# Kernel tuning notes

Hardware: AMD Instinct MI355X
Metric: run time of the kernel (lower is better)

Reference implementation:

```python
import jax, jax.numpy as jnp
import numpy as np

B, N, H = 32, 256, 1024
HEADS, NHID = 8, 128
NCLS = 7
BAND = 24
ALPHA = 0.2          # GAT leaky-relu slope
NEG = -9e15          # masked-attention fill, as in pyGAT


def setup_inputs() -> dict:
    key = jax.random.key(0)
    ks = jax.random.split(key, 16)
    def nrm(k, shp, s=0.02):
        return jax.random.normal(k, shp, dtype=jnp.float32) * s
    hidden_cls = jax.random.normal(ks[0], (B, N, H), dtype=jnp.float32)
    hidden_emo = jax.random.normal(ks[1], (B, N, H), dtype=jnp.float32)
    # causal band cliques, diagonal included (GAT uses clique - eye)
    t = jnp.arange(N)
    band = ((t[None, :] <= t[:, None]) & (t[None, :] > t[:, None] - BAND)).astype(jnp.float32)
    clique = jnp.broadcast_to(band, (B, N, N))
    labels = jax.random.randint(ks[2], (B, N), 0, NCLS)
    pooler_W = nrm(ks[3], (H, H)); pooler_b = jnp.zeros((H,), jnp.float32)
    gat_W = nrm(ks[4], (HEADS, H, NHID))
    gat_a1 = nrm(ks[5], (HEADS, NHID)); gat_a2 = nrm(ks[6], (HEADS, NHID))
    out_W = nrm(ks[7], (H, H))            # heads*nhid == H -> nclass=H
    out_a1 = nrm(ks[8], (H,)); out_a2 = nrm(ks[9], (H,))
    lin1_W = nrm(ks[10], (H, H)); lin1_b = jnp.zeros((H,), jnp.float32)
    lin0_W = nrm(ks[11], (2 * H, H)); lin0_b = jnp.zeros((H,), jnp.float32)
    cls_W = nrm(ks[12], (H, NCLS)); cls_b = jnp.zeros((NCLS,), jnp.float32)
    A = jax.random.uniform(ks[13], (NCLS, NCLS), dtype=jnp.float32) + 0.1
    hmm_A = A / A.sum(axis=1, keepdims=True)   # row-stochastic transition matrix
    return dict(hidden_cls=hidden_cls, hidden_emo=hidden_emo, clique=clique,
                labels=labels, pooler_W=pooler_W, pooler_b=pooler_b,
                gat_W=gat_W, gat_a1=gat_a1, gat_a2=gat_a2,
                out_W=out_W, out_a1=out_a1, out_a2=out_a2,
                lin1_W=lin1_W, lin1_b=lin1_b, lin0_W=lin0_W, lin0_b=lin0_b,
                cls_W=cls_W, cls_b=cls_b, hmm_A=hmm_A)


def _lrelu(x):
    return jnp.where(x > 0, x, ALPHA * x)


def reference(hidden_cls, hidden_emo, clique, labels, pooler_W, pooler_b,
              gat_W, gat_a1, gat_a2, out_W, out_a1, out_a2,
              lin1_W, lin1_b, lin0_W, lin0_b, cls_W, cls_b, hmm_A):
    # PoolerAll: dense + tanh on all token states (dropout = identity in eval)
    fea_cls = jnp.tanh(hidden_cls @ pooler_W + pooler_b)   # [B,N,H] (CLS per utt)
    fea_emo = jnp.tanh(hidden_emo @ pooler_W + pooler_b)   # [B,N,H] (mask tok per utt)

    eyeN = jnp.eye(N, dtype=clique.dtype)
    adjm = (clique - eyeN) > 0                             # [B,N,N] GAT adjacency

    def gat_one(x, am):                                    # x [N,H], am [N,N]
        Wh = jnp.einsum('nf,hfd->hnd', x, gat_W)           # [heads,N,nhid]
        e = _lrelu(jnp.einsum('hnd,hd->hn', Wh, gat_a1)[:, :, None]
                   + jnp.einsum('hnd,hd->hn', Wh, gat_a2)[:, None, :])
        att = jax.nn.softmax(jnp.where(am[None], e, NEG), axis=-1)
        h1 = jax.nn.elu(jnp.einsum('hnm,hmd->hnd', att, Wh))
        h1 = jnp.transpose(h1, (1, 0, 2)).reshape(N, HEADS * NHID)
        Wh2 = h1 @ out_W                                   # out attention layer (concat=False)
        e2 = _lrelu((Wh2 @ out_a1)[:, None] + (Wh2 @ out_a2)[None, :])
        h2 = jax.nn.softmax(jnp.where(am, e2, NEG), axis=-1) @ Wh2
        return jax.nn.elu(h2)                              # [N,H]

    gat_out = jax.vmap(gat_one)(fea_cls, adjm)             # [B,N,H]
    # row 0 replaced by (dropout of) fea_cls row 0, as in the original
    g = jnp.concatenate([fea_cls[:, :1], gat_out[:, 1:]], axis=1)
    g = jnp.concatenate([fea_cls, g @ lin1_W + lin1_b], axis=-1) @ lin0_W + lin0_b
    log_gat = jax.nn.softmax(g @ cls_W + cls_b, axis=-1)   # [B,N,NCLS] (probs)

    # HMM emission probs hmm_B(fea) = softmax(classifier(fea))
    Bprob = jax.nn.softmax(fea_emo @ cls_W + cls_b, axis=-1)  # [B,N,NCLS]
    P0 = jnp.full((NCLS,), 1.0 / NCLS, dtype=jnp.float32)
    AT = hmm_A.T

    def hmm_row(Bp, mrow):                                 # Bp [N,NCLS], mrow [N]
        def step(carry, xs):
            p, started = carry
            bt, m = xs
            p_init = P0 * bt; p_init = p_init / p_init.sum()
            p_tr = (AT @ p) * bt; p_tr = p_tr / p_tr.sum()
            p_new = jnp.where(started, p_tr, p_init)
            valid = m > 0.5
            return (jnp.where(valid, p_new, p), started | valid), None
        (p, _), _ = jax.lax.scan(step, (P0, jnp.asarray(False)), (Bp, mrow))
        return p                                           # final filtered posterior

    log_hmm = jax.vmap(lambda Bp, M: jax.vmap(lambda mr: hmm_row(Bp, mr))(M))(Bprob, clique)

    logits = jnp.log((log_gat + log_hmm) * 0.5).reshape(B * N, NCLS)
    lab = labels.reshape(B * N)
    mask = lab >= 0
    picked = jnp.take_along_axis(logits, jnp.where(mask, lab, 0)[:, None], axis=1)[:, 0]
    loss = -(jnp.where(mask, picked, 0.0).sum() / jnp.maximum(mask.sum(), 1).astype(jnp.float32))
    return loss, logits
```

## Files before the change

kernel.cpp:

```cpp
#include <hip/hip_runtime.h>
#include <hip/hip_bf16.h>
#include <math.h>

typedef __hip_bfloat16 bf16;
typedef __attribute__((ext_vector_type(8))) short short8;
typedef __attribute__((ext_vector_type(4))) float float4v;

static constexpr int Bb = 32, Nn = 256, Hh = 1024, HEADS = 8, NHID = 128, NCLS = 7, BAND = 24;
static constexpr int M = Bb * Nn;
static constexpr float ALPHA = 0.2f;
static constexpr long INEL = (long)M * Hh;

__device__ __forceinline__ float tof(bf16 x) { return __bfloat162float(x); }
__device__ __forceinline__ bf16 tob(float x) { return __float2bfloat16(x); }
__device__ __forceinline__ unsigned short f2bits(float x) {
    bf16 h = __float2bfloat16(x);
    return *(unsigned short*)&h;
}
__device__ __forceinline__ float bits2f(unsigned short u) {
    unsigned v = ((unsigned)u) << 16;
    float f;
    __builtin_memcpy(&f, &v, 4);
    return f;
}

__device__ __forceinline__ void gload16(const void* g, void* l) {
    __builtin_amdgcn_global_load_lds(
        (const __attribute__((address_space(1))) void*)g,
        (__attribute__((address_space(3))) void*)l, 16, 0, 0);
}

static constexpr long OFF_PWT  = 0;
static constexpr long OFF_PB   = 1048576;
static constexpr long OFF_WCT  = 1049600;
static constexpr long OFF_GA1  = 2098176;
static constexpr long OFF_GA2  = 2099200;
static constexpr long OFF_OWT  = 2100224;
static constexpr long OFF_OA1  = 3148800;
static constexpr long OFF_OA2  = 3149824;
static constexpr long OFF_CWT  = 6298624;
static constexpr long OFF_CB   = 6305792;
static constexpr long OFF_HA   = 6305799;
static constexpr long W_TOTAL  = 6305848;

__device__ __forceinline__ float ldany(const void* p, long i, int isb) {
    return isb ? tof(((const bf16*)p)[i]) : ((const float*)p)[i];
}

__global__ __launch_bounds__(256) void small_convert_k(
    const void* pW, const void* pb, const void* ga1, const void* ga2,
    const void* oa1, const void* oa2, const void* cW, const void* cb,
    const void* hA, bf16* __restrict__ dst, int* __restrict__ flag) {
    __shared__ int sb[256];
    const int t = threadIdx.x;
    int bad = 0;
    for (int i = t; i < 4096; i += 256) {
        float v = tof(((const bf16*)pW)[i]);
        if (!(fabsf(v) < 1e4f)) bad = 1;
    }
    sb[t] = bad; __syncthreads();
    for (int s = 128; s; s >>= 1) { if (t < s) sb[t] |= sb[t + s]; __syncthreads(); }
    const int isb = sb[0] ? 0 : 1;
    if (t == 0) *flag = isb;
    for (int i = t; i < 1024; i += 256) {
        dst[OFF_PB  + i] = tob(ldany(pb,  i, isb));
        dst[OFF_GA1 + i] = tob(ldany(ga1, i, isb));
        dst[OFF_GA2 + i] = tob(ldany(ga2, i, isb));
        dst[OFF_OA1 + i] = tob(ldany(oa1, i, isb));
        dst[OFF_OA2 + i] = tob(ldany(oa2, i, isb));
    }
    for (int i = t; i < 7168; i += 256) {
        int c = i >> 10, k = i & 1023;
        dst[OFF_CWT + i] = tob(ldany(cW, (long)k * 7 + c, isb));
    }
    if (t < NCLS) dst[OFF_CB + t] = tob(ldany(cb, t, isb));
    if (t < NCLS * NCLS) dst[OFF_HA + t] = tob(ldany(hA, t, isb));
}

__global__ __launch_bounds__(256) void transposeT_k(const int* __restrict__ flagp,
                                                    const void* __restrict__ pW,
                                                    const void* __restrict__ oW,
                                                    const void* __restrict__ gW,
                                                    bf16* __restrict__ dst) {
    __shared__ float S[64][65];
    const int isb = *flagp;
    const int z = blockIdx.z;
    const int tx = threadIdx.x, ty0 = threadIdx.y;
    if (z < 2) {
        const void* src = z ? oW : pW;
        const long doff = z ? OFF_OWT : OFF_PWT;
        const int r0 = blockIdx.y * 64, c0 = blockIdx.x * 64;
        #pragma unroll 4
        for (int it = 0; it < 16; ++it) {
            int ty = it * 4 + ty0;
            S[ty][tx] = ldany(src, (long)(r0 + ty) * 1024 + c0 + tx, isb);
        }
        __syncthreads();
        #pragma unroll 4
        for (int it = 0; it < 16; ++it) {
            int ty = it * 4 + ty0;
            dst[doff + (long)(c0 + ty) * 1024 + r0 + tx] = tob(S[tx][ty]);
        }
    } else {
        if (blockIdx.x >= 2) return;
        const int h = z - 2;
        const int r0 = blockIdx.y * 64, c0 = blockIdx.x * 64;
        const long sbase = (long)h * 131072;
        #pragma unroll 4
        for (int it = 0; it < 16; ++it) {
            int ty = it * 4 + ty0;
            S[ty][tx] = ldany(gW, sbase + (long)(r0 + ty) * 128 + c0 + tx, isb);
        }
        __syncthreads();
        #pragma unroll 4
        for (int it = 0; it < 16; ++it) {
            int ty = it * 4 + ty0;
            dst[OFF_WCT + (long)(h * 128 + c0 + ty) * 1024 + r0 + tx] = tob(S[tx][ty]);
        }
    }
}

__global__ void convin_k(const int* __restrict__ flagp, const void* __restrict__ s0,
                         const void* __restrict__ s1, bf16* __restrict__ d0,
                         bf16* __restrict__ d1) {
    const int isb = *flagp;
    if (isb) return;
    long i = ((long)blockIdx.x * 256 + threadIdx.x) * 8;
    const void* s; bf16* d; long off;
    if (i < INEL) { s = s0; d = d0; off = i; }
    else          { s = s1; d = d1; off = i - INEL; }
    const float* f = (const float*)s + off;
    unsigned short tmp[8];
    #pragma unroll
    for (int q = 0; q < 8; ++q) tmp[q] = f2bits(f[q]);
    *(int4*)(d + off) = *(int4*)tmp;
}

__global__ __launch_bounds__(256) void gvec_k(const int* __restrict__ flagp,
                                              const void* __restrict__ l0W,
                                              const void* __restrict__ cWr,
                                              float* __restrict__ W1T,
                                              float* __restrict__ Gb) {
    __shared__ float S[1024][NCLS];
    const int t = threadIdx.x;
    const int isb = *flagp;
    for (int j = t; j < 1024; j += 256) {
        #pragma unroll
        for (int c = 0; c < NCLS; ++c) S[j][c] = ldany(cWr, (long)j * 7 + c, isb);
    }
    __syncthreads();
    const int wave = t >> 6, lane = t & 63;
    #pragma unroll
    for (int r = 0; r < 2; ++r) {
        int k = blockIdx.x * 8 + wave * 2 + r;
        float acc[NCLS];
        #pragma unroll
        for (int c = 0; c < NCLS; ++c) acc[c] = 0.f;
        #pragma unroll
        for (int q = 0; q < 16; ++q) {
            int j = lane * 16 + q;
            float x = ldany(l0W, (long)k * 1024 + j, isb);
            #pragma unroll
            for (int c = 0; c < NCLS; ++c) acc[c] += x * S[j][c];
        }
        #pragma unroll
        for (int c = 0; c < NCLS; ++c)
            #pragma unroll
            for (int off = 32; off; off >>= 1) acc[c] += __shfl_down(acc[c], off);
        if (lane == 0) {
            #pragma unroll
            for (int c = 0; c < NCLS; ++c) {
                if (k < 1024) W1T[c * 1024 + k] = acc[c];
                else          Gb[(k - 1024) * 7 + c] = acc[c];
            }
        }
    }
}

__global__ __launch_bounds__(256) void w2_k(const int* __restrict__ flagp,
                                            const void* __restrict__ l1W,
                                            const float* __restrict__ Gb,
                                            float* __restrict__ W2T) {
    __shared__ float S[1024][NCLS];
    const int t = threadIdx.x;
    const int isb = *flagp;
    for (int j = t; j < 1024; j += 256) {
        #pragma unroll
        for (int c = 0; c < NCLS; ++c) S[j][c] = Gb[(long)j * 7 + c];
    }
    __syncthreads();
    const int wave = t >> 6, lane = t & 63;
    #pragma unroll
    for (int r = 0; r < 2; ++r) {
        int i = blockIdx.x * 8 + wave * 2 + r;
        float acc[NCLS];
        #pragma unroll
        for (int c = 0; c < NCLS; ++c) acc[c] = 0.f;
        #pragma unroll
        for (int q = 0; q < 16; ++q) {
            int o = lane * 16 + q;
            float x = ldany(l1W, (long)i * 1024 + o, isb);
            #pragma unroll
            for (int c = 0; c < NCLS; ++c) acc[c] += x * S[o][c];
        }
        #pragma unroll
        for (int c = 0; c < NCLS; ++c)
            #pragma unroll
            for (int off = 32; off; off >>= 1) acc[c] += __shfl_down(acc[c], off);
        if (lane == 0) {
            #pragma unroll
            for (int c = 0; c < NCLS; ++c) W2T[c * 1024 + i] = acc[c];
        }
    }
}

__global__ void cvec_k(const int* __restrict__ flagp, const void* __restrict__ l1b,
                       const void* __restrict__ l0b, const void* __restrict__ cWr,
                       const void* __restrict__ cbr, const float* __restrict__ Gb,
                       float* __restrict__ cvec) {
    int lane = threadIdx.x;
    int isb = *flagp;
    float acc[NCLS];
    #pragma unroll
    for (int c = 0; c < NCLS; ++c) acc[c] = 0.f;
    for (int o = lane; o < 1024; o += 64) {
        float b1 = ldany(l1b, o, isb);
        float b0 = ldany(l0b, o, isb);
        #pragma unroll
        for (int c = 0; c < NCLS; ++c)
            acc[c] += b1 * Gb[o * 7 + c] + b0 * ldany(cWr, (long)o * 7 + c, isb);
    }
    #pragma unroll
    for (int c = 0; c < NCLS; ++c)
        #pragma unroll
        for (int off = 32; off; off >>= 1) acc[c] += __shfl_down(acc[c], off);
    if (lane == 0) {
        #pragma unroll
        for (int c = 0; c < NCLS; ++c) cvec[c] = acc[c] + ldany(cbr, c, isb);
    }
}

static constexpr int SLOT_US = 256 * 32;

template <int ACT>
__device__ __forceinline__ void gemm_pipe_core(
    const bf16* __restrict__ A, int strideA,
    const bf16* __restrict__ Bt, int strideB,
    const bf16* __restrict__ bias, bf16* __restrict__ Cout,
    int Nc, int K, int bm, int bn, unsigned short* lds) {
    const int tid = threadIdx.x;
    const int lane = tid & 63;
    const int wave = tid >> 6;
    const int wm = (wave >> 1) * 64, wn = (wave & 1) * 64;
    const int l15 = lane & 15, quad = lane >> 4;
    const int csw = ((lane & 3) ^ ((lane >> 2) & 3) ^ (lane >> 4)) * 8;
    const int sc8 = (quad ^ (l15 & 3) ^ (l15 >> 2)) * 8;

    long aoff[2], boff[2];
    #pragma unroll
    for (int o = 0; o < 2; ++o) {
        aoff[o] = (long)(bm + wave * 32 + o * 16 + (lane >> 2)) * strideA + csw;
        boff[o] = (long)(bn + wave * 32 + o * 16 + (lane >> 2)) * strideB + csw;
    }
    const int aDst = wave * 32 * 32;
    const int bDst = (128 + wave * 32) * 32;

    const int nt = K / 32;
    float4v acc[4][4];
    #pragma unroll
    for (int i = 0; i < 4; ++i)
        #pragma unroll
        for (int j = 0; j < 4; ++j) acc[i][j] = (float4v){0.f, 0.f, 0.f, 0.f};

    auto stage = [&](int ts, int slot) {
        unsigned short* buf = lds + slot * SLOT_US;
        int k = ts * 32;
        gload16(A + aoff[0] + k, buf + aDst);
        gload16(A + aoff[1] + k, buf + aDst + 512);
        gload16(Bt + boff[0] + k, buf + bDst);
        gload16(Bt + boff[1] + k, buf + bDst + 512);
    };
    auto frags = [&](int slot, short8* af, short8* bfr) {
        const unsigned short* bufc = lds + slot * SLOT_US;
        #pragma unroll
        for (int i = 0; i < 4; ++i)
            af[i] = *(const short8*)(bufc + (wm + i * 16 + l15) * 32 + sc8);
        #pragma unroll
        for (int j = 0; j < 4; ++j)
            bfr[j] = *(const short8*)(bufc + (128 + wn + j * 16 + l15) * 32 + sc8);
    };

    stage(0, 0); stage(1, 1); stage(2, 2);
    asm volatile("s_waitcnt vmcnt(8)" ::: "memory");
    __builtin_amdgcn_s_barrier();
    asm volatile("" ::: "memory");
    short8 afA[4], bfA[4], afB[4], bfB[4];
    frags(0, afA, bfA);
    int c0 = 0, c1 = 1, c2 = 2;

    for (int t = 0; t < nt; t += 2) {
        asm volatile("s_waitcnt lgkmcnt(0)" ::: "memory");
        if (t < nt - 2) asm volatile("s_waitcnt vmcnt(4)" ::: "memory");
        else            asm volatile("s_waitcnt vmcnt(0)" ::: "memory");
        __builtin_amdgcn_s_barrier();
        asm volatile("" ::: "memory");
        if (t + 3 < nt) stage(t + 3, c0);
        if (t + 1 < nt) frags(c1, afB, bfB);
        __builtin_amdgcn_s_setprio(1);
        #pragma unroll
        for (int i = 0; i < 4; ++i)
            #pragma unroll
            for (int j = 0; j < 4; ++j)
                acc[i][j] = __builtin_amdgcn_mfma_f32_16x16x32_bf16(afA[i], bfA[j], acc[i][j], 0, 0, 0);
        __builtin_amdgcn_s_setprio(0);
        asm volatile("" ::: "memory");
        asm volatile("s_waitcnt lgkmcnt(0)" ::: "memory");
        if (t + 1 < nt - 2) asm volatile("s_waitcnt vmcnt(4)" ::: "memory");
        else                asm volatile("s_waitcnt vmcnt(0)" ::: "memory");
        __builtin_amdgcn_s_barrier();
        asm volatile("" ::: "memory");
        if (t + 4 < nt) stage(t + 4, c1);
        if (t + 2 < nt) frags(c2, afA, bfA);
        __builtin_amdgcn_s_setprio(1);
        #pragma unroll
        for (int i = 0; i < 4; ++i)
            #pragma unroll
            for (int j = 0; j < 4; ++j)
                acc[i][j] = __builtin_amdgcn_mfma_f32_16x16x32_bf16(afB[i], bfB[j], acc[i][j], 0, 0, 0);
        __builtin_amdgcn_s_setprio(0);
        asm volatile("" ::: "memory");
        int n0 = c2, n1 = c0, n2 = c1;
        c0 = n0; c1 = n1; c2 = n2;
    }

    #pragma unroll
    for (int j = 0; j < 4; ++j) {
        int gn = bn + wn + j * 16 + l15;
        float bj = bias ? tof(bias[gn]) : 0.f;
        #pragma unroll
        for (int i = 0; i < 4; ++i) {
            #pragma unroll
            for (int r = 0; r < 4; ++r) {
                int gm = bm + wm + i * 16 + quad * 4 + r;
                float v = acc[i][j][r] + bj;
                if (ACT == 1) v = tanhf(v);
                Cout[(long)gm * Nc + gn] = tob(v);
            }
        }
    }
}

template <int ACT>
__global__ __launch_bounds__(256, 3) void gemm_pipe_k(const bf16* __restrict__ A,
                                                      const bf16* __restrict__ Bt,
                                                      const bf16* __restrict__ bias,
                                                      bf16* __restrict__ Cout,
                                                      int Nc, int K) {
    __shared__ __align__(16) unsigned short lds[3 * SLOT_US];
    gemm_pipe_core<ACT>(A, K, Bt, K, bias, Cout, Nc, K,
                        blockIdx.x * 128, blockIdx.y * 128, lds);
}

__global__ __launch_bounds__(256, 3) void gemmP_pipe_k(const int* __restrict__ flagp,
                                                       const bf16* __restrict__ rawA,
                                                       const bf16* __restrict__ convA,
                                                       const bf16* __restrict__ Bt,
                                                       const bf16* __restrict__ bias,
                                                       bf16* __restrict__ Cout) {
    __shared__ __align__(16) unsigned short lds[3 * SLOT_US];
    const bf16* A = (*flagp) ? rawA : convA;
    gemm_pipe_core<1>(A, Hh, Bt, Hh, bias, Cout, Hh, Hh,
                      blockIdx.x * 128, blockIdx.y * 128, lds);
}

__global__ __launch_bounds__(256) void att1f_k(const bf16* __restrict__ Wh,
                                               const bf16* __restrict__ ga1,
                                               const bf16* __restrict__ ga2,
                                               bf16* __restrict__ h1) {
    const int bx = blockIdx.x;
    const int t = threadIdx.x;
    if (bx >= 512) {
        if (t < 64) {
            int bh = bx - 512;
            int h = bh & 7, b = bh >> 3;
            int lane = t;
            float s0 = 0.f, s1 = 0.f;
            long base = (long)(b * 256) * 1024 + h * 128 + lane * 2;
            for (int m = 0; m < 256; ++m) {
                unsigned u = *(const unsigned*)(Wh + base + (long)m * 1024);
                s0 += bits2f((unsigned short)(u & 0xffff));
                s1 += bits2f((unsigned short)(u >> 16));
            }
            s0 *= (1.0f / 256.0f); s1 *= (1.0f / 256.0f);
            s0 = s0 > 0.f ? s0 : expm1f(s0);
            s1 = s1 > 0.f ? s1 : expm1f(s1);
            unsigned out = (unsigned)f2bits(s0) | ((unsigned)f2bits(s1) << 16);
            *(unsigned*)(h1 + base) = out;
        }
        return;
    }
    __shared__ unsigned short S[152][128];
    __shared__ float f1s[152], f2s[152];
    __shared__ float att[128][25];
    const int b = bx >> 4, h = (bx >> 1) & 7, half = bx & 1;
    const int nbase = half * 128;
    const int mstart = half ? (nbase - (BAND - 1)) : 0;
    const int mcount = half ? (256 - mstart) : 128;
    const int c = t & 15;

    float av1[8], av2[8];
    {
        union { int4 v; unsigned short us[8]; } u1, u2;
        u1.v = *(const int4*)(ga1 + h * 128 + c * 8);
        u2.v = *(const int4*)(ga2 + h * 128 + c * 8);
        #pragma unroll
        for (int qq = 0; qq < 8; ++qq) { av1[qq] = bits2f(u1.us[qq]); av2[qq] = bits2f(u2.us[qq]); }
    }

    const int iters = (mcount * 16 + 255) >> 8;
    for (int i = 0; i < iters; ++i) {
        int li = i * 256 + t;
        int mr = li >> 4;
        if (mr < mcount) {
            long ga = (long)(b * 256 + mstart + mr) * 1024 + h * 128 + c * 8;
            union { int4 v; unsigned short us[8]; } u;
            u.v = *(const int4*)(Wh + ga);
            float p1 = 0.f, p2 = 0.f;
            #pragma unroll
            for (int qq = 0; qq < 8; ++qq) {
                float f = bits2f(u.us[qq]);
                p1 += f * av1[qq]; p2 += f * av2[qq];
            }
            *(int4*)&S[mr][c * 8] = u.v;
            #pragma unroll
            for (int mask = 1; mask < 16; mask <<= 1) {
                p1 += __shfl_xor(p1, mask);
                p2 += __shfl_xor(p2, mask);
            }
            if (c == 0) { f1s[mr] = p1; f2s[mr] = p2; }
        }
    }
    __syncthreads();

    if (t < 128) {
        int n = nbase + t;
        if (n > 0) {
            int cnt = n < (BAND - 1) ? n : (BAND - 1);
            int m0 = n - cnt;
            float f1n = f1s[n - mstart];
            float e[BAND - 1];
            float mx = -1e30f;
            for (int i = 0; i < cnt; ++i) {
                float v = f1n + f2s[m0 + i - mstart];
                v = v > 0.f ? v : ALPHA * v;
                e[i] = v; mx = fmaxf(mx, v);
            }
            float ss = 0.f;
            for (int i = 0; i < cnt; ++i) { e[i] = __expf(e[i] - mx); ss += e[i]; }
            float inv = 1.0f / ss;
            for (int i = 0; i < cnt; ++i) att[t][i] = e[i] * inv;
        }
    }
    __syncthreads();

    const int wave = t >> 6, lane = t & 63;
    for (int ln = wave; ln < 128; ln += 4) {
        int n = nbase + ln;
        if (n == 0) continue;
        int cnt = n < (BAND - 1) ? n : (BAND - 1);
        int mr0 = n - cnt - mstart;
        float s0 = 0.f, s1 = 0.f;
        for (int i = 0; i < cnt; ++i) {
            float a = att[ln][i];
            unsigned u = *(const unsigned*)&S[mr0 + i][lane * 2];
            s0 += a * bits2f((unsigned short)(u & 0xffff));
            s1 += a * bits2f((unsigned short)(u >> 16));
        }
        s0 = s0 > 0.f ? s0 : expm1f(s0);
        s1 = s1 > 0.f ? s1 : expm1f(s1);
        unsigned out = (unsigned)f2bits(s0) | ((unsigned)f2bits(s1) << 16);
        *(unsigned*)(h1 + (long)(b * 256 + n) * 1024 + h * 128 + lane * 2) = out;
    }
}

__global__ void f12b_k(const bf16* __restrict__ Wh2, const bf16* __restrict__ a1,
                       const bf16* __restrict__ a2, float* __restrict__ f1b,
                       float* __restrict__ f2b) {
    int idx = blockIdx.x;
    int lane = threadIdx.x;
    const bf16* row = Wh2 + (long)idx * 1024 + lane * 16;
    float s1 = 0.f, s2 = 0.f;
    #pragma unroll
    for (int half = 0; half < 2; ++half) {
        union { int4 v; unsigned short us[8]; } x, w1, w2;
        x.v  = *(const int4*)(row + half * 8);
        w1.v = *(const int4*)(a1 + lane * 16 + half * 8);
        w2.v = *(const int4*)(a2 + lane * 16 + half * 8);
        #pragma unroll
        for (int q = 0; q < 8; ++q) {
            float f = bits2f(x.us[q]);
            s1 += f * bits2f(w1.us[q]);
            s2 += f * bits2f(w2.us[q]);
        }
    }
    #pragma unroll
    for (int off = 32; off; off >>= 1) {
        s1 += __shfl_down(s1, off);
        s2 += __shfl_down(s2, off);
    }
    if (lane == 0) { f1b[idx] = s1; f2b[idx] = s2; }
}

__global__ __launch_bounds__(256) void att2f_k(const bf16* __restrict__ Wh2,
                                               const float* __restrict__ f1b,
                                               const float* __restrict__ f2b,
                                               bf16* __restrict__ g) {
    __shared__ unsigned short S[152][128];
    __shared__ float att[128][25];
    const int bx = blockIdx.x;
    const int b = bx >> 4, half = (bx >> 3) & 1, jt = bx & 7;
    const int nbase = half * 128;
    const int mstart = half ? (nbase - (BAND - 1)) : 0;
    const int mcount = half ? (256 - mstart) : 128;
    const int t = threadIdx.x;
    const int c = t & 15;

    const int iters = (mcount * 16 + 255) >> 8;
    for (int i = 0; i < iters; ++i) {
        int li = i * 256 + t;
        int mr = li >> 4;
        if (mr < mcount) {
            long ga = (long)(b * 256 + mstart + mr) * 1024 + jt * 128 + c * 8;
            *(int4*)&S[mr][c * 8] = *(const int4*)(Wh2 + ga);
        }
    }
    __syncthreads();

    if (t < 128) {
        int n = nbase + t;
        if (n > 0) {
            int cnt = n < (BAND - 1) ? n : (BAND - 1);
            int m0 = n - cnt;
            float f1n = f1b[b * 256 + n];
            float e[BAND - 1];
            float mx = -1e30f;
            for (int i = 0; i < cnt; ++i) {
                float v = f1n + f2b[b * 256 + m0 + i];
                v = v > 0.f ? v : ALPHA * v;
                e[i] = v; mx = fmaxf(mx, v);
            }
            float ss = 0.f;
            for (int i = 0; i < cnt; ++i) { e[i] = __expf(e[i] - mx); ss += e[i]; }
            float inv = 1.0f / ss;
            for (int i = 0; i < cnt; ++i) att[t][i] = e[i] * inv;
        }
    }
    __syncthreads();

    const int wave = t >> 6, lane = t & 63;
    for (int ln = wave; ln < 128; ln += 4) {
        int n = nbase + ln;
        if (n == 0) continue;
        int cnt = n < (BAND - 1) ? n : (BAND - 1);
        int mr0 = n - cnt - mstart;
        float s0 = 0.f, s1 = 0.f;
        for (int i = 0; i < cnt; ++i) {
            float a = att[ln][i];
            unsigned u = *(const unsigned*)&S[mr0 + i][lane * 2];
            s0 += a * bits2f((unsigned short)(u & 0xffff));
            s1 += a * bits2f((unsigned short)(u >> 16));
        }
        s0 = s0 > 0.f ? s0 : expm1f(s0);
        s1 = s1 > 0.f ? s1 : expm1f(s1);
        unsigned out = (unsigned)f2bits(s0) | ((unsigned)f2bits(s1) << 16);
        *(unsigned*)(g + (long)(b * 256 + n) * 1024 + jt * 128 + lane * 2) = out;
    }
}

__global__ void cls7_k(const bf16* __restrict__ X, const bf16* __restrict__ Wt,
                       const bf16* __restrict__ b, float* __restrict__ out, int K) {
    int row = blockIdx.x;
    int lane = threadIdx.x;
    float xv[16];
    {
        const bf16* x = X + (long)row * K + lane * 16;
        union { int4 v; unsigned short us[8]; } u0, u1;
        u0.v = *(const int4*)x; u1.v = *(const int4*)(x + 8);
        #pragma unroll
        for (int q = 0; q < 8; ++q) { xv[q] = bits2f(u0.us[q]); xv[q + 8] = bits2f(u1.us[q]); }
    }
    float acc[NCLS];
    #pragma unroll
    for (int cc = 0; cc < NCLS; ++cc) {
        const bf16* wr = Wt + (long)cc * K + lane * 16;
        union { int4 v; unsigned short us[8]; } w0, w1;
        w0.v = *(const int4*)wr; w1.v = *(const int4*)(wr + 8);
        float s = 0.f;
        #pragma unroll
        for (int q = 0; q < 8; ++q) {
            s += xv[q] * bits2f(w0.us[q]);
            s += xv[q + 8] * bits2f(w1.us[q]);
        }
        acc[cc] = s;
    }
    #pragma unroll
    for (int cc = 0; cc < NCLS; ++cc)
        #pragma unroll
        for (int off = 32; off; off >>= 1) acc[cc] += __shfl_down(acc[cc], off);
    if (lane == 0) {
        float mx = -1e30f;
        #pragma unroll
        for (int cc = 0; cc < NCLS; ++cc) { acc[cc] += tof(b[cc]); mx = fmaxf(mx, acc[cc]); }
        float s = 0.f;
        #pragma unroll
        for (int cc = 0; cc < NCLS; ++cc) { acc[cc] = expf(acc[cc] - mx); s += acc[cc]; }
        float inv = 1.0f / s;
        #pragma unroll
        for (int cc = 0; cc < NCLS; ++cc) out[(long)row * NCLS + cc] = acc[cc] * inv;
    }
}

__global__ void lgat2_k(const bf16* __restrict__ X, const bf16* __restrict__ Y,
                        const float* __restrict__ W1T, const float* __restrict__ W2T,
                        const float* __restrict__ cvec, float* __restrict__ out) {
    int row = blockIdx.x;
    int lane = threadIdx.x;
    const bf16* ybase = (row & 255) ? Y : X;
    float xv[16], yv[16];
    {
        const bf16* x = X + (long)row * 1024 + lane * 16;
        const bf16* y = ybase + (long)row * 1024 + lane * 16;
        union { int4 v; unsigned short us[8]; } u0, u1, v0, v1;
        u0.v = *(const int4*)x; u1.v = *(const int4*)(x + 8);
        v0.v = *(const int4*)y; v1.v = *(const int4*)(y + 8);
        #pragma unroll
        for (int q = 0; q < 8; ++q) {
            xv[q] = bits2f(u0.us[q]); xv[q + 8] = bits2f(u1.us[q]);
            yv[q] = bits2f(v0.us[q]); yv[q + 8] = bits2f(v1.us[q]);
        }
    }
    float acc[NCLS];
    #pragma unroll
    for (int cc = 0; cc < NCLS; ++cc) {
        const float4* w1 = (const float4*)(W1T + (long)cc * 1024 + lane * 16);
        const float4* w2 = (const float4*)(W2T + (long)cc * 1024 + lane * 16);
        float s = 0.f;
        #pragma unroll
        for (int h = 0; h < 4; ++h) {
            float4 a = w1[h], b = w2[h];
            s += xv[h * 4 + 0] * a.x + xv[h * 4 + 1] * a.y + xv[h * 4 + 2] * a.z + xv[h * 4 + 3] * a.w;
            s += yv[h * 4 + 0] * b.x + yv[h * 4 + 1] * b.y + yv[h * 4 + 2] * b.z + yv[h * 4 + 3] * b.w;
        }
        acc[cc] = s;
    }
    #pragma unroll
    for (int cc = 0; cc < NCLS; ++cc)
        #pragma unroll
        for (int off = 32; off; off >>= 1) acc[cc] += __shfl_down(acc[cc], off);
    if (lane == 0) {
        float mx = -1e30f;
        #pragma unroll
        for (int cc = 0; cc < NCLS; ++cc) { acc[cc] += cvec[cc]; mx = fmaxf(mx, acc[cc]); }
        float s = 0.f;
        #pragma unroll
        for (int cc = 0; cc < NCLS; ++cc) { acc[cc] = expf(acc[cc] - mx); s += acc[cc]; }
        float inv = 1.0f / s;
        #pragma unroll
        for (int cc = 0; cc < NCLS; ++cc) out[(long)row * NCLS + cc] = acc[cc] * inv;
    }
}

__global__ void hmm_k(const float* __restrict__ Bprob, const bf16* __restrict__ hmm_A,
                      float* __restrict__ out, float* __restrict__ loss_acc) {
    __shared__ float AT[NCLS][NCLS];
    int t = threadIdx.x;
    if (blockIdx.x == 0 && t == 0) *loss_acc = 0.f;
    if (t < NCLS * NCLS) {
        int i = t / NCLS, j = t % NCLS;
        AT[i][j] = tof(hmm_A[j * NCLS + i]);
    }
    __syncthreads();
    int idx = blockIdx.x * 64 + t;
    int n = idx & 255, b = idx >> 8;
    int t0 = n - (BAND - 1) > 0 ? n - (BAND - 1) : 0;
    const float* Bp = Bprob + (long)(b * 256) * NCLS;
    float p[NCLS];
    float s = 0.f;
    #pragma unroll
    for (int cc = 0; cc < NCLS; ++cc) { p[cc] = Bp[t0 * NCLS + cc]; s += p[cc]; }
    float inv = 1.0f / s;
    #pragma unroll
    for (int cc = 0; cc < NCLS; ++cc) p[cc] *= inv;
    for (int tt = t0 + 1; tt <= n; ++tt) {
        float q[NCLS]; float ss = 0.f;
        #pragma unroll
        for (int i = 0; i < NCLS; ++i) {
            float a = 0.f;
            #pragma unroll
            for (int j = 0; j < NCLS; ++j) a += AT[i][j] * p[j];
            a *= Bp[tt * NCLS + i];
            q[i] = a; ss += a;
        }
        float iv = 1.0f / ss;
        #pragma unroll
        for (int i = 0; i < NCLS; ++i) p[i] = q[i] * iv;
    }
    #pragma unroll
    for (int cc = 0; cc < NCLS; ++cc) out[(long)idx * NCLS + cc] = p[cc];
}

__global__ void final_k(const float* __restrict__ lg, const float* __restrict__ lh,
                        const int* __restrict__ labels, void* __restrict__ out,
                        float* __restrict__ loss_acc, const int* __restrict__ flagp) {
    int idx = blockIdx.x * blockDim.x + threadIdx.x;
    const int isb = *flagp;
    float lo[NCLS];
    int lab = labels[idx];
    #pragma unroll
    for (int c = 0; c < NCLS; ++c) {
        float v = logf(0.5f * (lg[(long)idx * NCLS + c] + lh[(long)idx * NCLS + c]));
        lo[c] = v;
        long o = 1 + (long)idx * NCLS + c;
        if (isb) ((bf16*)out)[o] = tob(v);
        else     ((float*)out)[o] = v;
    }
    float picked = lo[lab];
    __shared__ float red[256];
    red[threadIdx.x] = picked;
    __syncthreads();
    for (int s = 128; s; s >>= 1) {
        if (threadIdx.x < s) red[threadIdx.x] += red[threadIdx.x + s];
        __syncthreads();
    }
    if (threadIdx.x == 0) atomicAdd(loss_acc, red[0]);
}

__global__ void loss_k(const float* __restrict__ acc, void* __restrict__ out,
                       const int* __restrict__ flagp) {
    float v = -acc[0] / (float)(Bb * Nn);
    if (*flagp) ((bf16*)out)[0] = tob(v);
    else        ((float*)out)[0] = v;
}

extern "C" void kernel_launch(void* const* d_in, const int* in_sizes, int n_in,
                              void* d_out, int out_size, void* d_ws, size_t ws_size,
                              hipStream_t stream) {
    const void* hidden_cls = d_in[0];
    const void* hidden_emo = d_in[1];
    const int* labels = (const int*)d_in[3];

    char* w = (char*)d_ws;
    bf16* C  = (bf16*)w;
    bf16* E  = C + INEL;
    bf16* Wb = E + INEL;
    bf16* H2 = Wb + INEL;
    bf16* wc = H2 + INEL;
    float* f1b   = (float*)(wc + W_TOTAL);
    float* f2b   = f1b + M;
    float* Bprob = f2b + M;
    float* lgat  = Bprob + (long)M * NCLS;
    float* lhmm  = lgat + (long)M * NCLS;
    float* loss_acc = lhmm + (long)M * NCLS;
    int*   flag  = (int*)(loss_acc + 1);
    float* W1f   = (float*)(flag + 1);
    float* W2f   = W1f + 7 * 1024;
    float* Gbf   = W2f + 7 * 1024;
    float* cvec  = Gbf + 1024 * 7;

    dim3 gblk(256);
    dim3 ggrid(M / 128, Hh / 128);

    small_convert_k<<<1, 256, 0, stream>>>(d_in[4], d_in[5], d_in[7], d_in[8],
                                           d_in[10], d_in[11], d_in[16], d_in[17],
                                           d_in[18], wc, flag);
    transposeT_k<<<dim3(16, 16, 10), dim3(64, 4), 0, stream>>>(flag, d_in[4], d_in[9],
                                                               d_in[6], wc);
    gvec_k<<<256, 256, 0, stream>>>(flag, d_in[14], d_in[16], W1f, Gbf);
    w2_k<<<128, 256, 0, stream>>>(flag, d_in[12], Gbf, W2f);
    cvec_k<<<1, 64, 0, stream>>>(flag, d_in[13], d_in[15], d_in[16], d_in[17], Gbf, cvec);
    convin_k<<<(int)(2 * INEL / (256 * 8)), 256, 0, stream>>>(flag, hidden_emo, hidden_cls, Wb, H2);

    gemmP_pipe_k<<<ggrid, gblk, 0, stream>>>(flag, (const bf16*)hidden_emo, Wb,
                                             wc + OFF_PWT, wc + OFF_PB, E);
    gemmP_pipe_k<<<ggrid, gblk, 0, stream>>>(flag, (const bf16*)hidden_cls, H2,
                                             wc + OFF_PWT, wc + OFF_PB, C);
    cls7_k<<<M, 64, 0, stream>>>(E, wc + OFF_CWT, wc + OFF_CB, Bprob, Hh);
    gemm_pipe_k<0><<<ggrid, gblk, 0, stream>>>(C, wc + OFF_WCT, (const bf16*)nullptr, Wb, Hh, Hh);
    att1f_k<<<768, 256, 0, stream>>>(Wb, wc + OFF_GA1, wc + OFF_GA2, E);
    gemm_pipe_k<0><<<ggrid, gblk, 0, stream>>>(E, wc + OFF_OWT, (const bf16*)nullptr, Wb, Hh, Hh);
    f12b_k<<<M, 64, 0, stream>>>(Wb, wc + OFF_OA1, wc + OFF_OA2, f1b, f2b);
    att2f_k<<<512, 256, 0, stream>>>(Wb, f1b, f2b, E);
    lgat2_k<<<M, 64, 0, stream>>>(C, E, W1f, W2f, cvec, lgat);
    hmm_k<<<M / 64, 64, 0, stream>>>(Bprob, wc + OFF_HA, lhmm, loss_acc);
    final_k<<<M / 256, 256, 0, stream>>>(lgat, lhmm, labels, d_out, loss_acc, flag);
    loss_k<<<1, 1, 0, stream>>>(loss_acc, d_out, flag);
}
```

Measured before the change: 472.1 us.

## Merge prep, GEMM, classifier, HMM and loss kernels into fewer fused launches

Collapses the many small prep kernels (constant conversion, transposes, gvec, input conversion) into one multi-role prep1 kernel, and w2 plus cvec into prep2. The two pooler GEMMs run in one z=2 grid. The cls7 head is fused into the first GAT GEMM launch and the f1/f2 attention dots into the output GEMM epilogue via atomics. HMM is co-scheduled with att2, and logits, final and loss are merged using a last-block counter. This removes launch overhead and intermediate round trips, but every prep block now redundantly probes the dtype flag and the f1/f2 atomics add contention.

```diff
diff --git a/kernel.cpp b/kernel.cpp
--- a/kernel.cpp
+++ b/kernel.cpp
@@ -47,12 +47,7 @@
     return isb ? tof(((const bf16*)p)[i]) : ((const float*)p)[i];
 }
 
-__global__ __launch_bounds__(256) void small_convert_k(
-    const void* pW, const void* pb, const void* ga1, const void* ga2,
-    const void* oa1, const void* oa2, const void* cW, const void* cb,
-    const void* hA, bf16* __restrict__ dst, int* __restrict__ flag) {
-    __shared__ int sb[256];
-    const int t = threadIdx.x;
+__device__ __forceinline__ int probe_dev(const void* pW, int t, int* sb) {
     int bad = 0;
     for (int i = t; i < 4096; i += 256) {
         float v = tof(((const bf16*)pW)[i]);
@@ -60,75 +55,123 @@
     }
     sb[t] = bad; __syncthreads();
     for (int s = 128; s; s >>= 1) { if (t < s) sb[t] |= sb[t + s]; __syncthreads(); }
-    const int isb = sb[0] ? 0 : 1;
-    if (t == 0) *flag = isb;
-    for (int i = t; i < 1024; i += 256) {
-        dst[OFF_PB  + i] = tob(ldany(pb,  i, isb));
-        dst[OFF_GA1 + i] = tob(ldany(ga1, i, isb));
-        dst[OFF_GA2 + i] = tob(ldany(ga2, i, isb));
-        dst[OFF_OA1 + i] = tob(ldany(oa1, i, isb));
-        dst[OFF_OA2 + i] = tob(ldany(oa2, i, isb));
-    }
-    for (int i = t; i < 7168; i += 256) {
-        int c = i >> 10, k = i & 1023;
-        dst[OFF_CWT + i] = tob(ldany(cW, (long)k * 7 + c, isb));
-    }
-    if (t < NCLS) dst[OFF_CB + t] = tob(ldany(cb, t, isb));
-    if (t < NCLS * NCLS) dst[OFF_HA + t] = tob(ldany(hA, t, isb));
-}
-
-__global__ __launch_bounds__(256) void transposeT_k(const int* __restrict__ flagp,
-                                                    const void* __restrict__ pW,
-                                                    const void* __restrict__ oW,
-                                                    const void* __restrict__ gW,
-                                                    bf16* __restrict__ dst) {
-    __shared__ float S[64][65];
-    const int isb = *flagp;
-    const int z = blockIdx.z;
-    const int tx = threadIdx.x, ty0 = threadIdx.y;
-    if (z < 2) {
-        const void* src = z ? oW : pW;
-        const long doff = z ? OFF_OWT : OFF_PWT;
-        const int r0 = blockIdx.y * 64, c0 = blockIdx.x * 64;
-        #pragma unroll 4
-        for (int it = 0; it < 16; ++it) {
-            int ty = it * 4 + ty0;
-            S[ty][tx] = ldany(src, (long)(r0 + ty) * 1024 + c0 + tx, isb);
+    int isb = sb[0] ? 0 : 1;
+    __syncthreads();
+    return isb;
+}
+
+__global__ __launch_bounds__(256) void prep1_k(
+    const void* pW, const void* pb, const void* gW, const void* ga1,
+    const void* ga2, const void* oW, const void* oa1, const void* oa2,
+    const void* l0W, const void* cW, const void* cb, const void* hA,
+    const void* in_emo, const void* in_cls,
+    bf16* __restrict__ wc, int* __restrict__ flag,
+    float* __restrict__ W1T, float* __restrict__ Gb,
+    bf16* __restrict__ d0, bf16* __restrict__ d1) {
+    __shared__ float SM[7168];
+    const int bx = blockIdx.x;
+    const int t = threadIdx.x;
+    const int isb = probe_dev(pW, t, (int*)SM);
+
+    if (bx == 0) {
+        if (t == 0) *flag = isb;
+        for (int i = t; i < 1024; i += 256) {
+            wc[OFF_PB  + i] = tob(ldany(pb,  i, isb));
+            wc[OFF_GA1 + i] = tob(ldany(ga1, i, isb));
+            wc[OFF_GA2 + i] = tob(ldany(ga2, i, isb));
+            wc[OFF_OA1 + i] = tob(ldany(oa1, i, isb));
+            wc[OFF_OA2 + i] = tob(ldany(oa2, i, isb));
+        }
+        for (int i = t; i < 7168; i += 256) {
+            int c = i >> 10, k = i & 1023;
+            wc[OFF_CWT + i] = tob(ldany(cW, (long)k * 7 + c, isb));
+        }
+        if (t < NCLS) wc[OFF_CB + t] = tob(ldany(cb, t, isb));
+        if (t < NCLS * NCLS) wc[OFF_HA + t] = tob(ldany(hA, t, isb));
+        return;
+    }
+    if (bx < 1 + 2560) {
+        int bi = bx - 1;
+        int z = bi >> 8, rem = bi & 255;
+        int bxx = rem & 15, byy = rem >> 4;
+        float (*S)[65] = (float(*)[65])SM;
+        const int tx = t & 63, ty0 = t >> 6;
+        if (z < 2) {
+            const void* src = z ? oW : pW;
+            const long doff = z ? OFF_OWT : OFF_PWT;
+            const int r0 = byy * 64, c0 = bxx * 64;
+            #pragma unroll 4
+            for (int it = 0; it < 16; ++it) {
+                int ty = it * 4 + ty0;
+                S[ty][tx] = ldany(src, (long)(r0 + ty) * 1024 + c0 + tx, isb);
+            }
+            __syncthreads();
+            #pragma unroll 4
+            for (int it = 0; it < 16; ++it) {
+                int ty = it * 4 + ty0;
+                wc[doff + (long)(c0 + ty) * 1024 + r0 + tx] = tob(S[tx][ty]);
+            }
+        } else {
+            if (bxx >= 2) return;
+            const int h = z - 2;
+            const int r0 = byy * 64, c0 = bxx * 64;
+            const long sbase = (long)h * 131072;
+            #pragma unroll 4
+            for (int it = 0; it < 16; ++it) {
+                int ty = it * 4 + ty0;
+                S[ty][tx] = ldany(gW, sbase + (long)(r0 + ty) * 128 + c0 + tx, isb);
+            }
+            __syncthreads();
+            #pragma unroll 4
+            for (int it = 0; it < 16; ++it) {
+                int ty = it * 4 + ty0;
+                wc[OFF_WCT + (long)(h * 128 + c0 + ty) * 1024 + r0 + tx] = tob(S[tx][ty]);
+            }
+        }
+        return;
+    }
+    if (bx < 1 + 2560 + 256) {
+        int bi = bx - 2561;
+        float (*S)[NCLS] = (float(*)[NCLS])SM;
+        for (int j = t; j < 1024; j += 256) {
+            #pragma unroll
+            for (int c = 0; c < NCLS; ++c) S[j][c] = ldany(cW, (long)j * 7 + c, isb);
         }
         __syncthreads();
-        #pragma unroll 4
-        for (int it = 0; it < 16; ++it) {
-            int ty = it * 4 + ty0;
-            dst[doff + (long)(c0 + ty) * 1024 + r0 + tx] = tob(S[tx][ty]);
-        }
-    } else {
-        if (blockIdx.x >= 2) return;
-        const int h = z - 2;
-        const int r0 = blockIdx.y * 64, c0 = blockIdx.x * 64;
-        const long sbase = (long)h * 131072;
-        #pragma unroll 4
-        for (int it = 0; it < 16; ++it) {
-            int ty = it * 4 + ty0;
-            S[ty][tx] = ldany(gW, sbase + (long)(r0 + ty) * 128 + c0 + tx, isb);
-        }
-        __syncthreads();
-        #pragma unroll 4
-        for (int it = 0; it < 16; ++it) {
-            int ty = it * 4 + ty0;
-            dst[OFF_WCT + (long)(h * 128 + c0 + ty) * 1024 + r0 + tx] = tob(S[tx][ty]);
-        }
-    }
-}
-
-__global__ void convin_k(const int* __restrict__ flagp, const void* __restrict__ s0,
-                         const void* __restrict__ s1, bf16* __restrict__ d0,
-                         bf16* __restrict__ d1) {
-    const int isb = *flagp;
+        const int wave = t >> 6, lane = t & 63;
+        #pragma unroll
+        for (int r = 0; r < 2; ++r) {
+            int k = bi * 8 + wave * 2 + r;
+            float acc[NCLS];
+            #pragma unroll
+            for (int c = 0; c < NCLS; ++c) acc[c] = 0.f;
+            #pragma unroll
+            for (int q = 0; q < 16; ++q) {
+                int j = lane * 16 + q;
+                float x = ldany(l0W, (long)k * 1024 + j, isb);
+                #pragma unroll
+                for (int c = 0; c < NCLS; ++c) acc[c] += x * S[j][c];
+            }
+            #pragma unroll
+            for (int c = 0; c < NCLS; ++c)
+                #pragma unroll
+                for (int off = 32; off; off >>= 1) acc[c] += __shfl_down(acc[c], off);
+            if (lane == 0) {
+                #pragma unroll
+                for (int c = 0; c < NCLS; ++c) {
+                    if (k < 1024) W1T[c * 1024 + k] = acc[c];
+                    else          Gb[(k - 1024) * 7 + c] = acc[c];
+                }
+            }
+        }
+        return;
+    }
     if (isb) return;
-    long i = ((long)blockIdx.x * 256 + threadIdx.x) * 8;
+    long bi = bx - 2817;
+    long i = (bi * 256 + t) * 8;
     const void* s; bf16* d; long off;
-    if (i < INEL) { s = s0; d = d0; off = i; }
-    else          { s = s1; d = d1; off = i - INEL; }
+    if (i < INEL) { s = in_emo; d = d0; off = i; }
+    else          { s = in_cls; d = d1; off = i - INEL; }
     const float* f = (const float*)s + off;
     unsigned short tmp[8];
     #pragma unroll
@@ -136,90 +179,52 @@
     *(int4*)(d + off) = *(int4*)tmp;
 }
 
-__global__ __launch_bounds__(256) void gvec_k(const int* __restrict__ flagp,
-                                              const void* __restrict__ l0W,
-                                              const void* __restrict__ cWr,
-                                              float* __restrict__ W1T,
-                                              float* __restrict__ Gb) {
+__global__ __launch_bounds__(256) void prep2_k(const int* __restrict__ flagp,
+                                               const void* __restrict__ l1W,
+                                               const void* __restrict__ l1b,
+                                               const void* __restrict__ l0b,
+                                               const void* __restrict__ cW,
+                                               const void* __restrict__ cb,
+                                               const float* __restrict__ Gb,
+                                               float* __restrict__ W2T,
+                                               float* __restrict__ cvec) {
     __shared__ float S[1024][NCLS];
+    const int bx = blockIdx.x;
     const int t = threadIdx.x;
     const int isb = *flagp;
-    for (int j = t; j < 1024; j += 256) {
-        #pragma unroll
-        for (int c = 0; c < NCLS; ++c) S[j][c] = ldany(cWr, (long)j * 7 + c, isb);
-    }
-    __syncthreads();
-    const int wave = t >> 6, lane = t & 63;
-    #pragma unroll
-    for (int r = 0; r < 2; ++r) {
-        int k = blockIdx.x * 8 + wave * 2 + r;
-        float acc[NCLS];
-        #pragma unroll
-        for (int c = 0; c < NCLS; ++c) acc[c] = 0.f;
-        #pragma unroll
-        for (int q = 0; q < 16; ++q) {
-            int j = lane * 16 + q;
-            float x = ldany(l0W, (long)k * 1024 + j, isb);
-            #pragma unroll
-            for (int c = 0; c < NCLS; ++c) acc[c] += x * S[j][c];
-        }
-        #pragma unroll
-        for (int c = 0; c < NCLS; ++c)
-            #pragma unroll
-            for (int off = 32; off; off >>= 1) acc[c] += __shfl_down(acc[c], off);
-        if (lane == 0) {
-            #pragma unroll
-            for (int c = 0; c < NCLS; ++c) {
-                if (k < 1024) W1T[c * 1024 + k] = acc[c];
-                else          Gb[(k - 1024) * 7 + c] = acc[c];
-            }
-        }
-    }
-}
-
-__global__ __launch_bounds__(256) void w2_k(const int* __restrict__ flagp,
-                                            const void* __restrict__ l1W,
-                                            const float* __restrict__ Gb,
-                                            float* __restrict__ W2T) {
-    __shared__ float S[1024][NCLS];
-    const int t = threadIdx.x;
-    const int isb = *flagp;
-    for (int j = t; j < 1024; j += 256) {
-        #pragma unroll
-        for (int c = 0; c < NCLS; ++c) S[j][c] = Gb[(long)j * 7 + c];
-    }
-    __syncthreads();
-    const int wave = t >> 6, lane = t & 63;
-    #pragma unroll
-    for (int r = 0; r < 2; ++r) {
-        int i = blockIdx.x * 8 + wave * 2 + r;
-        float acc[NCLS];
-        #pragma unroll
-        for (int c = 0; c < NCLS; ++c) acc[c] = 0.f;
-        #pragma unroll
-        for (int q = 0; q < 16; ++q) {
-            int o = lane * 16 + q;
-            float x = ldany(l1W, (long)i * 1024 + o, isb);
-            #pragma unroll
-            for (int c = 0; c < NCLS; ++c) acc[c] += x * S[o][c];
-        }
-        #pragma unroll
-        for (int c = 0; c < NCLS; ++c)
-            #pragma unroll
-            for (int off = 32; off; off >>= 1) acc[c] += __shfl_down(acc[c], off);
-        if (lane == 0) {
-            #pragma unroll
-            for (int c = 0; c < NCLS; ++c) W2T[c * 1024 + i] = acc[c];
-        }
-    }
-}
-
-__global__ void cvec_k(const int* __restrict__ flagp, const void* __restrict__ l1b,
-                       const void* __restrict__ l0b, const void* __restrict__ cWr,
-                       const void* __restrict__ cbr, const float* __restrict__ Gb,
-                       float* __restrict__ cvec) {
-    int lane = threadIdx.x;
-    int isb = *flagp;
+    if (bx < 128) {
+        for (int j = t; j < 1024; j += 256) {
+            #pragma unroll
+            for (int c = 0; c < NCLS; ++c) S[j][c] = Gb[(long)j * 7 + c];
+        }
+        __syncthreads();
+        const int wave = t >> 6, lane = t & 63;
+        #pragma unroll
+        for (int r = 0; r < 2; ++r) {
+            int i = bx * 8 + wave * 2 + r;
+            float acc[NCLS];
+            #pragma unroll
+            for (int c = 0; c < NCLS; ++c) acc[c] = 0.f;
+            #pragma unroll
+            for (int q = 0; q < 16; ++q) {
+                int o = lane * 16 + q;
+                float x = ldany(l1W, (long)i * 1024 + o, isb);
+                #pragma unroll
+                for (int c = 0; c < NCLS; ++c) acc[c] += x * S[o][c];
+            }
+            #pragma unroll
+            for (int c = 0; c < NCLS; ++c)
+                #pragma unroll
+                for (int off = 32; off; off >>= 1) acc[c] += __shfl_down(acc[c], off);
+            if (lane == 0) {
+                #pragma unroll
+                for (int c = 0; c < NCLS; ++c) W2T[c * 1024 + i] = acc[c];
+            }
+        }
+        return;
+    }
+    if (t >= 64) return;
+    int lane = t;
     float acc[NCLS];
     #pragma unroll
     for (int c = 0; c < NCLS; ++c) acc[c] = 0.f;
@@ -228,7 +233,7 @@
         float b0 = ldany(l0b, o, isb);
         #pragma unroll
         for (int c = 0; c < NCLS; ++c)
-            acc[c] += b1 * Gb[o * 7 + c] + b0 * ldany(cWr, (long)o * 7 + c, isb);
+            acc[c] += b1 * Gb[o * 7 + c] + b0 * ldany(cW, (long)o * 7 + c, isb);
     }
     #pragma unroll
     for (int c = 0; c < NCLS; ++c)
@@ -236,18 +241,20 @@
         for (int off = 32; off; off >>= 1) acc[c] += __shfl_down(acc[c], off);
     if (lane == 0) {
         #pragma unroll
-        for (int c = 0; c < NCLS; ++c) cvec[c] = acc[c] + ldany(cbr, c, isb);
+        for (int c = 0; c < NCLS; ++c) cvec[c] = acc[c] + ldany(cb, c, isb);
     }
 }
 
 static constexpr int SLOT_US = 256 * 32;
 
-template <int ACT>
+template <int ACT, int DOTS>
 __device__ __forceinline__ void gemm_pipe_core(
     const bf16* __restrict__ A, int strideA,
     const bf16* __restrict__ Bt, int strideB,
     const bf16* __restrict__ bias, bf16* __restrict__ Cout,
-    int Nc, int K, int bm, int bn, unsigned short* lds) {
+    int Nc, int K, int bm, int bn, unsigned short* lds,
+    const bf16* __restrict__ oa1 = nullptr, const bf16* __restrict__ oa2 = nullptr,
+    float* __restrict__ f1b = nullptr, float* __restrict__ f2b = nullptr) {
     const int tid = threadIdx.x;
     const int lane = tid & 63;
     const int wave = tid >> 6;
@@ -348,49 +355,144 @@
             }
         }
     }
-}
-
-template <int ACT>
-__global__ __launch_bounds__(256, 3) void gemm_pipe_k(const bf16* __restrict__ A,
-                                                      const bf16* __restrict__ Bt,
-                                                      const bf16* __restrict__ bias,
-                                                      bf16* __restrict__ Cout,
-                                                      int Nc, int K) {
-    __shared__ __align__(16) unsigned short lds[3 * SLOT_US];
-    gemm_pipe_core<ACT>(A, K, Bt, K, bias, Cout, Nc, K,
-                        blockIdx.x * 128, blockIdx.y * 128, lds);
+    if (DOTS) {
+        float o1v[4], o2v[4];
+        #pragma unroll
+        for (int j = 0; j < 4; ++j) {
+            int gn = bn + wn + j * 16 + l15;
+            o1v[j] = tof(oa1[gn]); o2v[j] = tof(oa2[gn]);
+        }
+        #pragma unroll
+        for (int i = 0; i < 4; ++i) {
+            #pragma unroll
+            for (int r = 0; r < 4; ++r) {
+                int gm = bm + wm + i * 16 + quad * 4 + r;
+                float p1 = 0.f, p2 = 0.f;
+                #pragma unroll
+                for (int j = 0; j < 4; ++j) {
+                    float v = bits2f(f2bits(acc[i][j][r]));
+                    p1 += v * o1v[j]; p2 += v * o2v[j];
+                }
+                #pragma unroll
+                for (int m = 1; m < 16; m <<= 1) {
+                    p1 += __shfl_xor(p1, m); p2 += __shfl_xor(p2, m);
+                }
+                if (l15 == 0) { atomicAdd(&f1b[gm], p1); atomicAdd(&f2b[gm], p2); }
+            }
+        }
+    }
 }
 
 __global__ __launch_bounds__(256, 3) void gemmP_pipe_k(const int* __restrict__ flagp,
-                                                       const bf16* __restrict__ rawA,
-                                                       const bf16* __restrict__ convA,
+                                                       const bf16* __restrict__ rawE,
+                                                       const bf16* __restrict__ rawC,
+                                                       const bf16* __restrict__ A0,
+                                                       const bf16* __restrict__ A1,
                                                        const bf16* __restrict__ Bt,
                                                        const bf16* __restrict__ bias,
-                                                       bf16* __restrict__ Cout) {
+                                                       bf16* __restrict__ C0,
+                                                       bf16* __restrict__ C1) {
     __shared__ __align__(16) unsigned short lds[3 * SLOT_US];
-    const bf16* A = (*flagp) ? rawA : convA;
-    gemm_pipe_core<1>(A, Hh, Bt, Hh, bias, Cout, Hh, Hh,
-                      blockIdx.x * 128, blockIdx.y * 128, lds);
+    const int isb = *flagp;
+    const bf16* A = blockIdx.z ? (isb ? rawC : A1) : (isb ? rawE : A0);
+    bf16* C = blockIdx.z ? C1 : C0;
+    gemm_pipe_core<1, 0>(A, Hh, Bt, Hh, bias, C, Hh, Hh,
+                         blockIdx.x * 128, blockIdx.y * 128, lds);
+}
+
+__global__ __launch_bounds__(256, 3) void gemm_cls_k(const bf16* __restrict__ A,
+                                                     const bf16* __restrict__ Bt,
+                                                     bf16* __restrict__ Cout,
+                                                     const bf16* __restrict__ X,
+                                                     const bf16* __restrict__ Wt,
+                                                     const bf16* __restrict__ cb,
+                                                     float* __restrict__ Bout) {
+    __shared__ __align__(16) unsigned short lds[3 * SLOT_US];
+    const int bx = blockIdx.x;
+    if (bx < 512) {
+        gemm_pipe_core<0, 0>(A, Hh, Bt, Hh, (const bf16*)nullptr, Cout, Hh, Hh,
+                             (bx & 63) * 128, (bx >> 6) * 128, lds);
+        return;
+    }
+    const int t = threadIdx.x, wave = t >> 6, lane = t & 63;
+    const int row = (bx - 512) * 4 + wave;
+    float xv[16];
+    {
+        const bf16* x = X + (long)row * Hh + lane * 16;
+        union { int4 v; unsigned short us[8]; } u0, u1;
+        u0.v = *(const int4*)x; u1.v = *(const int4*)(x + 8);
+        #pragma unroll
+        for (int q = 0; q < 8; ++q) { xv[q] = bits2f(u0.us[q]); xv[q + 8] = bits2f(u1.us[q]); }
+    }
+    float acc[NCLS];
+    #pragma unroll
+    for (int cc = 0; cc < NCLS; ++cc) {
+        const bf16* wr = Wt + (long)cc * Hh + lane * 16;
+        union { int4 v; unsigned short us[8]; } w0, w1;
+        w0.v = *(const int4*)wr; w1.v = *(const int4*)(wr + 8);
+        float s = 0.f;
+        #pragma unroll
+        for (int q = 0; q < 8; ++q) {
+            s += xv[q] * bits2f(w0.us[q]);
+            s += xv[q + 8] * bits2f(w1.us[q]);
+        }
+        acc[cc] = s;
+    }
+    #pragma unroll
+    for (int cc = 0; cc < NCLS; ++cc)
+        #pragma unroll
+        for (int off = 32; off; off >>= 1) acc[cc] += __shfl_down(acc[cc], off);
+    if (lane == 0) {
+        float mx = -1e30f;
+        #pragma unroll
+        for (int cc = 0; cc < NCLS; ++cc) { acc[cc] += tof(cb[cc]); mx = fmaxf(mx, acc[cc]); }
+        float s = 0.f;
+        #pragma unroll
+        for (int cc = 0; cc < NCLS; ++cc) { acc[cc] = expf(acc[cc] - mx); s += acc[cc]; }
+        float inv = 1.0f / s;
+        #pragma unroll
+        for (int cc = 0; cc < NCLS; ++cc) Bout[(long)row * NCLS + cc] = acc[cc] * inv;
+    }
+}
+
+__global__ __launch_bounds__(256, 3) void gemm_f12_k(const bf16* __restrict__ A,
+                                                     const bf16* __restrict__ Bt,
+                                                     bf16* __restrict__ Cout,
+                                                     const bf16* __restrict__ oa1,
+                                                     const bf16* __restrict__ oa2,
+                                                     float* __restrict__ f1b,
+                                                     float* __restrict__ f2b) {
+    __shared__ __align__(16) unsigned short lds[3 * SLOT_US];
+    gemm_pipe_core<0, 1>(A, Hh, Bt, Hh, (const bf16*)nullptr, Cout, Hh, Hh,
+                         blockIdx.x * 128, blockIdx.y * 128, lds, oa1, oa2, f1b, f2b);
 }
 
 __global__ __launch_bounds__(256) void att1f_k(const bf16* __restrict__ Wh,
                                                const bf16* __restrict__ ga1,
                                                const bf16* __restrict__ ga2,
                                                bf16* __restrict__ h1) {
+    __shared__ unsigned short S[152][128];
+    __shared__ float f1s[152], f2s[152];
+    __shared__ float att[128][25];
     const int bx = blockIdx.x;
     const int t = threadIdx.x;
-    if (bx >= 512) {
-        if (t < 64) {
-            int bh = bx - 512;
-            int h = bh & 7, b = bh >> 3;
-            int lane = t;
-            float s0 = 0.f, s1 = 0.f;
-            long base = (long)(b * 256) * 1024 + h * 128 + lane * 2;
-            for (int m = 0; m < 256; ++m) {
-                unsigned u = *(const unsigned*)(Wh + base + (long)m * 1024);
-                s0 += bits2f((unsigned short)(u & 0xffff));
-                s1 += bits2f((unsigned short)(u >> 16));
-            }
+    const int wave = t >> 6, lane = t & 63;
+    if (bx < 256) {
+        int h = bx & 7, b = bx >> 3;
+        float s0 = 0.f, s1 = 0.f;
+        long base = (long)(b * 256) * 1024 + h * 128 + lane * 2;
+        for (int m = wave * 64; m < wave * 64 + 64; ++m) {
+            unsigned u = *(const unsigned*)(Wh + base + (long)m * 1024);
+            s0 += bits2f((unsigned short)(u & 0xffff));
+            s1 += bits2f((unsigned short)(u >> 16));
+        }
+        float* red = (float*)S;
+        red[(wave * 64 + lane) * 2]     = s0;
+        red[(wave * 64 + lane) * 2 + 1] = s1;
+        __syncthreads();
+        if (wave == 0) {
+            s0 = red[lane * 2] + red[(64 + lane) * 2] + red[(128 + lane) * 2] + red[(192 + lane) * 2];
+            s1 = red[lane * 2 + 1] + red[(64 + lane) * 2 + 1] + red[(128 + lane) * 2 + 1] + red[(192 + lane) * 2 + 1];
             s0 *= (1.0f / 256.0f); s1 *= (1.0f / 256.0f);
             s0 = s0 > 0.f ? s0 : expm1f(s0);
             s1 = s1 > 0.f ? s1 : expm1f(s1);
@@ -399,10 +501,8 @@
         }
         return;
     }
-    __shared__ unsigned short S[152][128];
-    __shared__ float f1s[152], f2s[152];
-    __shared__ float att[128][25];
-    const int b = bx >> 4, h = (bx >> 1) & 7, half = bx & 1;
+    const int bxm = bx - 256;
+    const int b = bxm >> 4, h = (bxm >> 1) & 7, half = bxm & 1;
     const int nbase = half * 128;
     const int mstart = half ? (nbase - (BAND - 1)) : 0;
     const int mcount = half ? (256 - mstart) : 128;
@@ -463,6 +563,110 @@
     }
     __syncthreads();
 
+    for (int ln = wave; ln < 128; ln += 4) {
+        int n = nbase + ln;
+        if (n == 0) continue;
+        int cnt = n < (BAND - 1) ? n : (BAND - 1);
+        int mr0 = n - cnt - mstart;
+        float s0 = 0.f, s1 = 0.f;
+        for (int i = 0; i < cnt; ++i) {
+            float a = att[ln][i];
+            unsigned u = *(const unsigned*)&S[mr0 + i][lane * 2];
+            s0 += a * bits2f((unsigned short)(u & 0xffff));
+            s1 += a * bits2f((unsigned short)(u >> 16));
+        }
+        s0 = s0 > 0.f ? s0 : expm1f(s0);
+        s1 = s1 > 0.f ? s1 : expm1f(s1);
+        unsigned out = (unsigned)f2bits(s0) | ((unsigned)f2bits(s1) << 16);
+        *(unsigned*)(h1 + (long)(b * 256 + n) * 1024 + h * 128 + lane * 2) = out;
+    }
+}
+
+__global__ __launch_bounds__(256) void att2f_hmm_k(const bf16* __restrict__ Wh2,
+                                                   const float* __restrict__ f1b,
+                                                   const float* __restrict__ f2b,
+                                                   bf16* __restrict__ g,
+                                                   const float* __restrict__ Bprob,
+                                                   const bf16* __restrict__ hmm_A,
+                                                   float* __restrict__ lhmm) {
+    __shared__ unsigned short S[152][128];
+    __shared__ float att[128][25];
+    __shared__ float AT[NCLS][NCLS];
+    const int bx = blockIdx.x;
+    const int t = threadIdx.x;
+    if (bx >= 512) {
+        if (t < NCLS * NCLS) {
+            int i = t / NCLS, j = t % NCLS;
+            AT[i][j] = tof(hmm_A[j * NCLS + i]);
+        }
+        __syncthreads();
+        int idx = (bx - 512) * 256 + t;
+        int n = idx & 255, b = idx >> 8;
+        int t0 = n - (BAND - 1) > 0 ? n - (BAND - 1) : 0;
+        const float* Bp = Bprob + (long)(b * 256) * NCLS;
+        float p[NCLS];
+        float s = 0.f;
+        #pragma unroll
+        for (int cc = 0; cc < NCLS; ++cc) { p[cc] = Bp[t0 * NCLS + cc]; s += p[cc]; }
+        float inv = 1.0f / s;
+        #pragma unroll
+        for (int cc = 0; cc < NCLS; ++cc) p[cc] *= inv;
+        for (int tt = t0 + 1; tt <= n; ++tt) {
+            float q[NCLS]; float ss = 0.f;
+            #pragma unroll
+            for (int i = 0; i < NCLS; ++i) {
+                float a = 0.f;
+                #pragma unroll
+                for (int j = 0; j < NCLS; ++j) a += AT[i][j] * p[j];
+                a *= Bp[tt * NCLS + i];
+                q[i] = a; ss += a;
+            }
+            float iv = 1.0f / ss;
+            #pragma unroll
+            for (int i = 0; i < NCLS; ++i) p[i] = q[i] * iv;
+        }
+        #pragma unroll
+        for (int cc = 0; cc < NCLS; ++cc) lhmm[(long)idx * NCLS + cc] = p[cc];
+        return;
+    }
+    const int b = bx >> 4, half = (bx >> 3) & 1, jt = bx & 7;
+    const int nbase = half * 128;
+    const int mstart = half ? (nbase - (BAND - 1)) : 0;
+    const int mcount = half ? (256 - mstart) : 128;
+    const int c = t & 15;
+
+    const int iters = (mcount * 16 + 255) >> 8;
+    for (int i = 0; i < iters; ++i) {
+        int li = i * 256 + t;
+        int mr = li >> 4;
+        if (mr < mcount) {
+            long ga = (long)(b * 256 + mstart + mr) * 1024 + jt * 128 + c * 8;
+            *(int4*)&S[mr][c * 8] = *(const int4*)(Wh2 + ga);
+        }
+    }
+    __syncthreads();
+
+    if (t < 128) {
+        int n = nbase + t;
+        if (n > 0) {
+            int cnt = n < (BAND - 1) ? n : (BAND - 1);
+            int m0 = n - cnt;
+            float f1n = f1b[b * 256 + n];
+            float e[BAND - 1];
+            float mx = -1e30f;
+            for (int i = 0; i < cnt; ++i) {
+                float v = f1n + f2b[b * 256 + m0 + i];
+                v = v > 0.f ? v : ALPHA * v;
+                e[i] = v; mx = fmaxf(mx, v);
+            }
+            float ss = 0.f;
+            for (int i = 0; i < cnt; ++i) { e[i] = __expf(e[i] - mx); ss += e[i]; }
+            float inv = 1.0f / ss;
+            for (int i = 0; i < cnt; ++i) att[t][i] = e[i] * inv;
+        }
+    }
+    __syncthreads();
+
     const int wave = t >> 6, lane = t & 63;
     for (int ln = wave; ln < 128; ln += 4) {
         int n = nbase + ln;
@@ -479,152 +683,25 @@
         s0 = s0 > 0.f ? s0 : expm1f(s0);
         s1 = s1 > 0.f ? s1 : expm1f(s1);
         unsigned out = (unsigned)f2bits(s0) | ((unsigned)f2bits(s1) << 16);
-        *(unsigned*)(h1 + (long)(b * 256 + n) * 1024 + h * 128 + lane * 2) = out;
-    }
-}
-
-__global__ void f12b_k(const bf16* __restrict__ Wh2, const bf16* __restrict__ a1,
-                       const bf16* __restrict__ a2, float* __restrict__ f1b,
-                       float* __restrict__ f2b) {
-    int idx = blockIdx.x;
-    int lane = threadIdx.x;
-    const bf16* row = Wh2 + (long)idx * 1024 + lane * 16;
-    float s1 = 0.f, s2 = 0.f;
-    #pragma unroll
-    for (int half = 0; half < 2; ++half) {
-        union { int4 v; unsigned short us[8]; } x, w1, w2;
-        x.v  = *(const int4*)(row + half * 8);
-        w1.v = *(const int4*)(a1 + lane * 16 + half * 8);
-        w2.v = *(const int4*)(a2 + lane * 16 + half * 8);
-        #pragma unroll
-        for (int q = 0; q < 8; ++q) {
-            float f = bits2f(x.us[q]);
-            s1 += f * bits2f(w1.us[q]);
-            s2 += f * bits2f(w2.us[q]);
-        }
-    }
-    #pragma unroll
-    for (int off = 32; off; off >>= 1) {
-        s1 += __shfl_down(s1, off);
-        s2 += __shfl_down(s2, off);
-    }
-    if (lane == 0) { f1b[idx] = s1; f2b[idx] = s2; }
-}
-
-__global__ __launch_bounds__(256) void att2f_k(const bf16* __restrict__ Wh2,
-                                               const float* __restrict__ f1b,
-                                               const float* __restrict__ f2b,
-                                               bf16* __restrict__ g) {
-    __shared__ unsigned short S[152][128];
-    __shared__ float att[128][25];
-    const int bx = blockIdx.x;
-    const int b = bx >> 4, half = (bx >> 3) & 1, jt = bx & 7;
-    const int nbase = half * 128;
-    const int mstart = half ? (nbase - (BAND - 1)) : 0;
-    const int mcount = half ? (256 - mstart) : 128;
-    const int t = threadIdx.x;
-    const int c = t & 15;
-
-    const int iters = (mcount * 16 + 255) >> 8;
-    for (int i = 0; i < iters; ++i) {
-        int li = i * 256 + t;
-        int mr = li >> 4;
-        if (mr < mcount) {
-            long ga = (long)(b * 256 + mstart + mr) * 1024 + jt * 128 + c * 8;
-            *(int4*)&S[mr][c * 8] = *(const int4*)(Wh2 + ga);
-        }
-    }
-    __syncthreads();
-
-    if (t < 128) {
-        int n = nbase + t;
-        if (n > 0) {
-            int cnt = n < (BAND - 1) ? n : (BAND - 1);
-            int m0 = n - cnt;
-            float f1n = f1b[b * 256 + n];
-            float e[BAND - 1];
-            float mx = -1e30f;
-            for (int i = 0; i < cnt; ++i) {
-                float v = f1n + f2b[b * 256 + m0 + i];
-                v = v > 0.f ? v : ALPHA * v;
-                e[i] = v; mx = fmaxf(mx, v);
-            }
-            float ss = 0.f;
-            for (int i = 0; i < cnt; ++i) { e[i] = __expf(e[i] - mx); ss += e[i]; }
-            float inv = 1.0f / ss;
-            for (int i = 0; i < cnt; ++i) att[t][i] = e[i] * inv;
-        }
-    }
-    __syncthreads();
-
-    const int wave = t >> 6, lane = t & 63;
-    for (int ln = wave; ln < 128; ln += 4) {
-        int n = nbase + ln;
-        if (n == 0) continue;
-        int cnt = n < (BAND - 1) ? n : (BAND - 1);
-        int mr0 = n - cnt - mstart;
-        float s0 = 0.f, s1 = 0.f;
-        for (int i = 0; i < cnt; ++i) {
-            float a = att[ln][i];
-            unsigned u = *(const unsigned*)&S[mr0 + i][lane * 2];
-            s0 += a * bits2f((unsigned short)(u & 0xffff));
-            s1 += a * bits2f((unsigned short)(u >> 16));
-        }
-        s0 = s0 > 0.f ? s0 : expm1f(s0);
-        s1 = s1 > 0.f ? s1 : expm1f(s1);
-        unsigned out = (unsigned)f2bits(s0) | ((unsigned)f2bits(s1) << 16);
         *(unsigned*)(g + (long)(b * 256 + n) * 1024 + jt * 128 + lane * 2) = out;
     }
 }
 
-__global__ void cls7_k(const bf16* __restrict__ X, const bf16* __restrict__ Wt,
-                       const bf16* __restrict__ b, float* __restrict__ out, int K) {
-    int row = blockIdx.x;
-    int lane = threadIdx.x;
-    float xv[16];
-    {
-        const bf16* x = X + (long)row * K + lane * 16;
-        union { int4 v; unsigned short us[8]; } u0, u1;
-        u0.v = *(const int4*)x; u1.v = *(const int4*)(x + 8);
-        #pragma unroll
-        for (int q = 0; q < 8; ++q) { xv[q] = bits2f(u0.us[q]); xv[q + 8] = bits2f(u1.us[q]); }
-    }
-    float acc[NCLS];
-    #pragma unroll
-    for (int cc = 0; cc < NCLS; ++cc) {
-        const bf16* wr = Wt + (long)cc * K + lane * 16;
-        union { int4 v; unsigned short us[8]; } w0, w1;
-        w0.v = *(const int4*)wr; w1.v = *(const int4*)(wr + 8);
-        float s = 0.f;
-        #pragma unroll
-        for (int q = 0; q < 8; ++q) {
-            s += xv[q] * bits2f(w0.us[q]);
-            s += xv[q + 8] * bits2f(w1.us[q]);
-        }
-        acc[cc] = s;
-    }
-    #pragma unroll
-    for (int cc = 0; cc < NCLS; ++cc)
-        #pragma unroll
-        for (int off = 32; off; off >>= 1) acc[cc] += __shfl_down(acc[cc], off);
-    if (lane == 0) {
-        float mx = -1e30f;
-        #pragma unroll
-        for (int cc = 0; cc < NCLS; ++cc) { acc[cc] += tof(b[cc]); mx = fmaxf(mx, acc[cc]); }
-        float s = 0.f;
-        #pragma unroll
-        for (int cc = 0; cc < NCLS; ++cc) { acc[cc] = expf(acc[cc] - mx); s += acc[cc]; }
-        float inv = 1.0f / s;
-        #pragma unroll
-        for (int cc = 0; cc < NCLS; ++cc) out[(long)row * NCLS + cc] = acc[cc] * inv;
-    }
-}
-
-__global__ void lgat2_k(const bf16* __restrict__ X, const bf16* __restrict__ Y,
-                        const float* __restrict__ W1T, const float* __restrict__ W2T,
-                        const float* __restrict__ cvec, float* __restrict__ out) {
-    int row = blockIdx.x;
-    int lane = threadIdx.x;
+__global__ __launch_bounds__(256) void lgf_k(const bf16* __restrict__ X,
+                                             const bf16* __restrict__ Y,
+                                             const float* __restrict__ W1T,
+                                             const float* __restrict__ W2T,
+                                             const float* __restrict__ cvec,
+                                             const float* __restrict__ lhmm,
+                                             const int* __restrict__ labels,
+                                             void* __restrict__ out,
+                                             float* __restrict__ loss_acc,
+                                             unsigned* __restrict__ counter,
+                                             const int* __restrict__ flagp) {
+    __shared__ float ps[4];
+    const int t = threadIdx.x, wave = t >> 6, lane = t & 63;
+    const int row = blockIdx.x * 4 + wave;
+    const int isb = *flagp;
     const bf16* ybase = (row & 255) ? Y : X;
     float xv[16], yv[16];
     {
@@ -665,81 +742,31 @@
         #pragma unroll
         for (int cc = 0; cc < NCLS; ++cc) { acc[cc] = expf(acc[cc] - mx); s += acc[cc]; }
         float inv = 1.0f / s;
-        #pragma unroll
-        for (int cc = 0; cc < NCLS; ++cc) out[(long)row * NCLS + cc] = acc[cc] * inv;
-    }
-}
-
-__global__ void hmm_k(const float* __restrict__ Bprob, const bf16* __restrict__ hmm_A,
-                      float* __restrict__ out, float* __restrict__ loss_acc) {
-    __shared__ float AT[NCLS][NCLS];
-    int t = threadIdx.x;
-    if (blockIdx.x == 0 && t == 0) *loss_acc = 0.f;
-    if (t < NCLS * NCLS) {
-        int i = t / NCLS, j = t % NCLS;
-        AT[i][j] = tof(hmm_A[j * NCLS + i]);
+        int lab = labels[row];
+        float picked = 0.f;
+        #pragma unroll
+        for (int cc = 0; cc < NCLS; ++cc) {
+            float pg = acc[cc] * inv;
+            float v = logf(0.5f * (pg + lhmm[(long)row * NCLS + cc]));
+            long o = 1 + (long)row * NCLS + cc;
+            if (isb) ((bf16*)out)[o] = tob(v);
+            else     ((float*)out)[o] = v;
+            if (cc == lab) picked = v;
+        }
+        ps[wave] = picked;
     }
     __syncthreads();
-    int idx = blockIdx.x * 64 + t;
-    int n = idx & 255, b = idx >> 8;
-    int t0 = n - (BAND - 1) > 0 ? n - (BAND - 1) : 0;
-    const float* Bp = Bprob + (long)(b * 256) * NCLS;
-    float p[NCLS];
-    float s = 0.f;
-    #pragma unroll
-    for (int cc = 0; cc < NCLS; ++cc) { p[cc] = Bp[t0 * NCLS + cc]; s += p[cc]; }
-    float inv = 1.0f / s;
-    #pragma unroll
-    for (int cc = 0; cc < NCLS; ++cc) p[cc] *= inv;
-    for (int tt = t0 + 1; tt <= n; ++tt) {
-        float q[NCLS]; float ss = 0.f;
-        #pragma unroll
-        for (int i = 0; i < NCLS; ++i) {
-            float a = 0.f;
-            #pragma unroll
-            for (int j = 0; j < NCLS; ++j) a += AT[i][j] * p[j];
-            a *= Bp[tt * NCLS + i];
-            q[i] = a; ss += a;
-        }
-        float iv = 1.0f / ss;
-        #pragma unroll
-        for (int i = 0; i < NCLS; ++i) p[i] = q[i] * iv;
-    }
-    #pragma unroll
-    for (int cc = 0; cc < NCLS; ++cc) out[(long)idx * NCLS + cc] = p[cc];
-}
-
-__global__ void final_k(const float* __restrict__ lg, const float* __restrict__ lh,
-                        const int* __restrict__ labels, void* __restrict__ out,
-                        float* __restrict__ loss_acc, const int* __restrict__ flagp) {
-    int idx = blockIdx.x * blockDim.x + threadIdx.x;
-    const int isb = *flagp;
-    float lo[NCLS];
-    int lab = labels[idx];
-    #pragma unroll
-    for (int c = 0; c < NCLS; ++c) {
-        float v = logf(0.5f * (lg[(long)idx * NCLS + c] + lh[(long)idx * NCLS + c]));
-        lo[c] = v;
-        long o = 1 + (long)idx * NCLS + c;
-        if (isb) ((bf16*)out)[o] = tob(v);
-        else     ((float*)out)[o] = v;
-    }
-    float picked = lo[lab];
-    __shared__ float red[256];
-    red[threadIdx.x] = picked;
-    __syncthreads();
-    for (int s = 128; s; s >>= 1) {
-        if (threadIdx.x < s) red[threadIdx.x] += red[threadIdx.x + s];
-        __syncthreads();
-    }
-    if (threadIdx.x == 0) atomicAdd(loss_acc, red[0]);
-}
-
-__global__ void loss_k(const float* __restrict__ acc, void* __restrict__ out,
-                       const int* __restrict__ flagp) {
-    float v = -acc[0] / (float)(Bb * Nn);
-    if (*flagp) ((bf16*)out)[0] = tob(v);
-    else        ((float*)out)[0] = v;
+    if (t == 0) {
+        atomicAdd(loss_acc, ps[0] + ps[1] + ps[2] + ps[3]);
+        __threadfence();
+        unsigned old = atomicAdd(counter, 1u);
+        if (old == gridDim.x - 1) {
+            float total = atomicAdd(loss_acc, 0.f);
+            float v = -total / (float)(Bb * Nn);
+            if (isb) ((bf16*)out)[0] = tob(v);
+            else     ((float*)out)[0] = v;
+        }
+    }
 }
 
 extern "C" void kernel_launch(void* const* d_in, const int* in_sizes, int n_in,
@@ -755,43 +782,37 @@
     bf16* Wb = E + INEL;
     bf16* H2 = Wb + INEL;
     bf16* wc = H2 + INEL;
-    float* f1b   = (float*)(wc + W_TOTAL);
-    float* f2b   = f1b + M;
-    float* Bprob = f2b + M;
-    float* lgat  = Bprob + (long)M * NCLS;
-    float* lhmm  = lgat + (long)M * NCLS;
-    float* loss_acc = lhmm + (long)M * NCLS;
-    int*   flag  = (int*)(loss_acc + 1);
-    float* W1f   = (float*)(flag + 1);
+    float* f1b      = (float*)(wc + W_TOTAL);
+    float* f2b      = f1b + M;
+    float* loss_acc = f2b + M;
+    unsigned* counter = (unsigned*)(loss_acc + 1);
+    int*   flag  = (int*)(counter + 1);
+    float* Bprob = (float*)(flag + 1);
+    float* lhmm  = Bprob + (long)M * NCLS;
+    float* W1f   = lhmm + (long)M * NCLS;
     float* W2f   = W1f + 7 * 1024;
     float* Gbf   = W2f + 7 * 1024;
     float* cvec  = Gbf + 1024 * 7;
 
     dim3 gblk(256);
-    dim3 ggrid(M / 128, Hh / 128);
-
-    small_convert_k<<<1, 256, 0, stream>>>(d_in[4], d_in[5], d_in[7], d_in[8],
-                                           d_in[10], d_in[11], d_in[16], d_in[17],
-                                           d_in[18], wc, flag);
-    transposeT_k<<<dim3(16, 16, 10), dim3(64, 4), 0, stream>>>(flag, d_in[4], d_in[9],
-                                                               d_in[6], wc);
-    gvec_k<<<256, 256, 0, stream>>>(flag, d_in[14], d_in[16], W1f, Gbf);
-    w2_k<<<128, 256, 0, stream>>>(flag, d_in[12], Gbf, W2f);
-    cvec_k<<<1, 64, 0, stream>>>(flag, d_in[13], d_in[15], d_in[16], d_in[17], Gbf, cvec);
-    convin_k<<<(int)(2 * INEL / (256 * 8)), 256, 0, stream>>>(flag, hidden_emo, hidden_cls, Wb, H2);
-
-    gemmP_pipe_k<<<ggrid, gblk, 0, stream>>>(flag, (const bf16*)hidden_emo, Wb,
-                                             wc + OFF_PWT, wc + OFF_PB, E);
-    gemmP_pipe_k<<<ggrid, gblk, 0, stream>>>(flag, (const bf16*)hidden_cls, H2,
-                                             wc + OFF_PWT, wc + OFF_PB, C);
-    cls7_k<<<M, 64, 0, stream>>>(E, wc + OFF_CWT, wc + OFF_CB, Bprob, Hh);
-    gemm_pipe_k<0><<<ggrid, gblk, 0, stream>>>(C, wc + OFF_WCT, (const bf16*)nullptr, Wb, Hh, Hh);
-    att1f_k<<<768, 256, 0, stream>>>(Wb, wc + OFF_GA1, wc + OFF_GA2, E);
-    gemm_pipe_k<0><<<ggrid, gblk, 0, stream>>>(E, wc + OFF_OWT, (const bf16*)nullptr, Wb, Hh, Hh);
-    f12b_k<<<M, 64, 0, stream>>>(Wb, wc + OFF_OA1, wc + OFF_OA2, f1b, f2b);
-    att2f_k<<<512, 256, 0, stream>>>(Wb, f1b, f2b, E);
-    lgat2_k<<<M, 64, 0, stream>>>(C, E, W1f, W2f, cvec, lgat);
-    hmm_k<<<M / 64, 64, 0, stream>>>(Bprob, wc + OFF_HA, lhmm, loss_acc);
-    final_k<<<M / 256, 256, 0, stream>>>(lgat, lhmm, labels, d_out, loss_acc, flag);
-    loss_k<<<1, 1, 0, stream>>>(loss_acc, d_out, flag);
-}
+
+    prep1_k<<<11009, gblk, 0, stream>>>(
+        d_in[4], d_in[5], d_in[6], d_in[7], d_in[8], d_in[9], d_in[10], d_in[11],
+        d_in[14], d_in[16], d_in[17], d_in[18], hidden_emo, hidden_cls,
+        wc, flag, W1f, Gbf, Wb, H2);
+    prep2_k<<<129, gblk, 0, stream>>>(flag, d_in[12], d_in[13], d_in[15],
+                                      d_in[16], d_in[17], Gbf, W2f, cvec);
+    gemmP_pipe_k<<<dim3(64, 8, 2), gblk, 0, stream>>>(
+        flag, (const bf16*)hidden_emo, (const bf16*)hidden_cls, Wb, H2,
+        wc + OFF_PWT, wc + OFF_PB, E, C);
+    gemm_cls_k<<<512 + 2048, gblk, 0, stream>>>(C, wc + OFF_WCT, Wb,
+                                                E, wc + OFF_CWT, wc + OFF_CB, Bprob);
+    att1f_k<<<768, gblk, 0, stream>>>(Wb, wc + OFF_GA1, wc + OFF_GA2, E);
+    (void)hipMemsetAsync(f1b, 0, (size_t)(2 * M + 2) * 4, stream);
+    gemm_f12_k<<<dim3(64, 8), gblk, 0, stream>>>(E, wc + OFF_OWT, Wb,
+                                                 wc + OFF_OA1, wc + OFF_OA2, f1b, f2b);
+    att2f_hmm_k<<<512 + 32, gblk, 0, stream>>>(Wb, f1b, f2b, E,
+                                               Bprob, wc + OFF_HA, lhmm);
+    lgf_k<<<2048, gblk, 0, stream>>>(C, E, W1f, W2f, cvec, lhmm, labels,
+                                     d_out, loss_acc, counter, flag);
+}
```

After: 515.2 us. +9.1%, slower.
